# Kernel tuning notes

Measured on AMD Instinct MI355X. Metric: run time of the kernel, lower is better.

The kernel has to match this reference:

```python
import jax, jax.numpy as jnp
import numpy as np

T, B, D, H = 128, 64, 1024, 1024

def hard_sigmoid(x):
    # torch: clamp(x + 0.5, 0, 1)
    return jnp.clip(x + 0.5, 0.0, 1.0)

def hard_tanh(x):
    # torch F.hardtanh default: clamp(x, -1, 1)
    return jnp.clip(x, -1.0, 1.0)

def setup_inputs() -> dict:
    key = jax.random.key(0)
    k1, k2, k3 = jax.random.split(key, 3)
    scale = 1.0 / np.sqrt(H)
    x = jax.random.normal(k1, (T, B, D), dtype=jnp.float32)
    Wx = jax.random.normal(k2, (D, 4 * H), dtype=jnp.float32) * scale
    Wh = jax.random.normal(k3, (H, 4 * H), dtype=jnp.float32) * scale
    b = jnp.zeros((4 * H,), dtype=jnp.float32)
    return {"x": x, "Wx": Wx, "Wh": Wh, "b": b}

def reference(x, Wx, Wh, b):
    # Hard-LSTM cell unrolled over time (dim 0), state carried via lax.scan.
    Bsz = x.shape[1]
    Hd = Wh.shape[0]

    def step(carry, xt):
        h, c = carry
        gates = xt @ Wx + h @ Wh + b          # [B, 4H]
        i, f, g, o = jnp.split(gates, 4, axis=-1)
        i = hard_sigmoid(i)
        f = hard_sigmoid(f)
        g = hard_tanh(g)
        o = hard_sigmoid(o)
        c_new = f * c + i * g
        h_new = o * hard_tanh(c_new)
        return (h_new, c_new), h_new

    h0 = jnp.zeros((Bsz, Hd), dtype=x.dtype)
    c0 = jnp.zeros((Bsz, Hd), dtype=x.dtype)
    _, hs = jax.lax.scan(step, (h0, c0), x)   # hs: [T, B, H]
    return hs
```

## Files before the change

### kernel.cpp

```cpp
#include <hip/hip_runtime.h>

#define TT 128
#define BB 64
#define DD 1024
#define HH 1024
#define G4 4096
#define MM (TT*BB)
#define BH (BB*HH)

#define NWG 256
#define RPAD 520

typedef float f32x4 __attribute__((ext_vector_type(4)));

__device__ __forceinline__ float hsig(float x) {
    x += 0.5f;
    return fminf(fmaxf(x, 0.0f), 1.0f);
}
__device__ __forceinline__ float htanh(float x) {
    return fminf(fmaxf(x, -1.0f), 1.0f);
}

__global__ void zero_bar(unsigned* p) {
    p[threadIdx.x] = 0u;
}

__global__ __launch_bounds__(256) void gx_gemm(const float* __restrict__ X,
                                               const float* __restrict__ W,
                                               const float* __restrict__ bias,
                                               float* __restrict__ C) {
    __shared__ float As[16][132];
    __shared__ float Bs[16][132];

    const int tid = threadIdx.x;
    const int tx = tid & 15;
    const int ty = tid >> 4;
    const int m0 = blockIdx.y * 128;
    const int n0 = blockIdx.x * 128;

    float acc[8][8] = {};
    float4 ra[2], rb[2];

    #pragma unroll
    for (int i = 0; i < 2; ++i) {
        int f4 = tid + i * 256;
        ra[i] = *(const float4*)(X + (size_t)(m0 + (f4 >> 2)) * DD + (f4 & 3) * 4);
        rb[i] = *(const float4*)(W + (size_t)(f4 >> 5) * G4 + n0 + (f4 & 31) * 4);
    }

    for (int k0 = 0; k0 < DD; k0 += 16) {
        #pragma unroll
        for (int i = 0; i < 2; ++i) {
            int f4 = tid + i * 256;
            int mi = f4 >> 2, kq = f4 & 3;
            As[kq * 4 + 0][mi] = ra[i].x;
            As[kq * 4 + 1][mi] = ra[i].y;
            As[kq * 4 + 2][mi] = ra[i].z;
            As[kq * 4 + 3][mi] = ra[i].w;
            *(float4*)&Bs[f4 >> 5][(f4 & 31) * 4] = rb[i];
        }
        __syncthreads();

        const int kn = (k0 + 16 < DD) ? (k0 + 16) : k0;
        #pragma unroll
        for (int i = 0; i < 2; ++i) {
            int f4 = tid + i * 256;
            ra[i] = *(const float4*)(X + (size_t)(m0 + (f4 >> 2)) * DD + kn + (f4 & 3) * 4);
            rb[i] = *(const float4*)(W + (size_t)(kn + (f4 >> 5)) * G4 + n0 + (f4 & 31) * 4);
        }

        #pragma unroll
        for (int kk = 0; kk < 16; ++kk) {
            float ar[8], br[8];
            *(float4*)&ar[0] = *(const float4*)&As[kk][ty * 4];
            *(float4*)&ar[4] = *(const float4*)&As[kk][64 + ty * 4];
            *(float4*)&br[0] = *(const float4*)&Bs[kk][tx * 4];
            *(float4*)&br[4] = *(const float4*)&Bs[kk][64 + tx * 4];
            #pragma unroll
            for (int i = 0; i < 8; ++i)
                #pragma unroll
                for (int j = 0; j < 8; ++j)
                    acc[i][j] += ar[i] * br[j];
        }
        __syncthreads();
    }

    float bl[8];
    *(float4*)&bl[0] = *(const float4*)(bias + n0 + tx * 4);
    *(float4*)&bl[4] = *(const float4*)(bias + n0 + 64 + tx * 4);
    #pragma unroll
    for (int i = 0; i < 8; ++i) {
        int mrow = m0 + ty * 4 + (i & 3) + 64 * (i >> 2);
        float* crow = C + (size_t)mrow * G4 + n0;
        float4 o1, o2;
        o1.x = acc[i][0] + bl[0]; o1.y = acc[i][1] + bl[1];
        o1.z = acc[i][2] + bl[2]; o1.w = acc[i][3] + bl[3];
        o2.x = acc[i][4] + bl[4]; o2.y = acc[i][5] + bl[5];
        o2.z = acc[i][6] + bl[6]; o2.w = acc[i][7] + bl[7];
        *(float4*)(crow + tx * 4) = o1;
        *(float4*)(crow + 64 + tx * 4) = o2;
    }
}

__global__ __launch_bounds__(512) void lstm_persist(const float* __restrict__ Gx,
                                                    const float* __restrict__ Wh,
                                                    float* __restrict__ out,
                                                    unsigned* __restrict__ flags) {
    __shared__ float smem[16640 + 1024];
    float* hs   = smem;
    float* red  = smem;
    float* gsum = smem + 16640;

    const int tid   = threadIdx.x;
    const int btile = blockIdx.x >> 5;
    const int hct   = blockIdx.x & 31;
    const int b0  = btile * 8;
    const int hc0 = hct * 32;

    const int kc = tid >> 4;
    const int tt = tid & 15;
    const int gate_m = tt >> 2;
    const int sub8 = (tt & 3) * 8;
    const float* wbase = Wh + (size_t)(kc * 32) * G4 + gate_m * HH + hc0 + sub8;

    const int pp  = tid >> 4;
    const int ss  = tid & 15;
    const int srow = ss >> 1;
    const int cq0  = (ss & 1) * 4;

    const bool cell_act = (tid < 256);
    const int cb  = tid >> 5;
    const int chc = tid & 31;
    const size_t cell_g = (size_t)(b0 + cb) * G4 + hc0 + chc;
    const size_t cell_h = (size_t)(b0 + cb) * HH + hc0 + chc;
    float creg = 0.0f;

    const int rb_ = tid >> 7;
    const int rgc = tid & 127;
    const int rtt = rgc >> 3;
    const int rj  = rgc & 7;

    unsigned* gflags = flags + btile * 32;

    if (cell_act) {
        const float* gr = Gx + cell_g;
        float ii = hsig(gr[0]);
        float gv = htanh(gr[2 * HH]);
        float oo = hsig(gr[3 * HH]);
        creg = ii * gv;
        __hip_atomic_store(out + cell_h, oo * htanh(creg),
                           __ATOMIC_RELAXED, __HIP_MEMORY_SCOPE_AGENT);
    }
    asm volatile("s_waitcnt vmcnt(0)" ::: "memory");
    __syncthreads();
    if (tid == 0)
        __hip_atomic_store(gflags + hct, 1u, __ATOMIC_RELAXED,
                           __HIP_MEMORY_SCOPE_AGENT);

    for (int t = 1; t < TT; ++t) {
        float gi = 0.f, gf = 0.f, gg = 0.f, go = 0.f;
        if (cell_act) {
            const float* gr = Gx + (size_t)t * BB * G4 + cell_g;
            gi = gr[0];
            gf = gr[HH];
            gg = gr[2 * HH];
            go = gr[3 * HH];
        }

        {
            while (__hip_atomic_load(gflags + pp, __ATOMIC_RELAXED,
                                     __HIP_MEMORY_SCOPE_AGENT) < (unsigned)t)
                __builtin_amdgcn_s_sleep(1);

            const float* hp = out + (size_t)(t - 1) * BH
                            + (size_t)(b0 + srow) * HH + pp * 32 + cq0 * 4;
            f32x4 v0, v1, v2, v3;
            asm volatile(
                "global_load_dwordx4 %0, %4, off sc0\n\t"
                "global_load_dwordx4 %1, %4, off offset:16 sc0\n\t"
                "global_load_dwordx4 %2, %4, off offset:32 sc0\n\t"
                "global_load_dwordx4 %3, %4, off offset:48 sc0\n\t"
                "s_waitcnt vmcnt(0)"
                : "=&v"(v0), "=&v"(v1), "=&v"(v2), "=&v"(v3)
                : "v"(hp)
                : "memory");
            float* hd = &hs[srow * 1152 + pp * 36 + cq0 * 4];
            *(f32x4*)(hd)      = v0;
            *(f32x4*)(hd + 4)  = v1;
            *(f32x4*)(hd + 8)  = v2;
            *(f32x4*)(hd + 12) = v3;
        }
        __syncthreads();

        float acc[8][8] = {};
        const float* wp = wbase;
        #pragma unroll 2
        for (int k4 = 0; k4 < 8; ++k4) {
            f32x4 hv[8];
            #pragma unroll
            for (int bi = 0; bi < 8; ++bi)
                hv[bi] = *(const f32x4*)&hs[bi * 1152 + kc * 36 + k4 * 4];
            #pragma unroll
            for (int j = 0; j < 4; ++j) {
                f32x4 w0 = *(const f32x4*)(wp);
                f32x4 w1 = *(const f32x4*)(wp + 4);
                wp += G4;
                #pragma unroll
                for (int bi = 0; bi < 8; ++bi) {
                    float h = hv[bi][j];
                    acc[bi][0] += h * w0[0];
                    acc[bi][1] += h * w0[1];
                    acc[bi][2] += h * w0[2];
                    acc[bi][3] += h * w0[3];
                    acc[bi][4] += h * w1[0];
                    acc[bi][5] += h * w1[1];
                    acc[bi][6] += h * w1[2];
                    acc[bi][7] += h * w1[3];
                }
            }
        }
        __syncthreads();

        #pragma unroll
        for (int round = 0; round < 2; ++round) {
            #pragma unroll
            for (int bi = 0; bi < 4; ++bi)
                #pragma unroll
                for (int j = 0; j < 8; ++j)
                    red[(size_t)(bi * 8 + j) * RPAD + tid] = acc[round * 4 + bi][j];
            __syncthreads();
            {
                const float* rp = red + (size_t)(rb_ * 8 + rj) * RPAD + rtt;
                float s0 = 0.f, s1 = 0.f, s2 = 0.f, s3 = 0.f;
                #pragma unroll
                for (int k2 = 0; k2 < 32; k2 += 4) {
                    s0 += rp[(k2 + 0) * 16];
                    s1 += rp[(k2 + 1) * 16];
                    s2 += rp[(k2 + 2) * 16];
                    s3 += rp[(k2 + 3) * 16];
                }
                gsum[(round * 4 + rb_) * 128 + rgc] = (s0 + s1) + (s2 + s3);
            }
            __syncthreads();
        }

        if (cell_act) {
            float ii = hsig(gi + gsum[cb * 128 + chc]);
            float ff = hsig(gf + gsum[cb * 128 + 32 + chc]);
            float gv = htanh(gg + gsum[cb * 128 + 64 + chc]);
            float oo = hsig(go + gsum[cb * 128 + 96 + chc]);
            creg = ff * creg + ii * gv;
            __hip_atomic_store(out + (size_t)t * BH + cell_h, oo * htanh(creg),
                               __ATOMIC_RELAXED, __HIP_MEMORY_SCOPE_AGENT);
        }
        asm volatile("s_waitcnt vmcnt(0)" ::: "memory");
        __syncthreads();
        if (tid == 0)
            __hip_atomic_store(gflags + hct, (unsigned)(t + 1),
                               __ATOMIC_RELAXED, __HIP_MEMORY_SCOPE_AGENT);
    }
}

extern "C" void kernel_launch(void* const* d_in, const int* in_sizes, int n_in,
                              void* d_out, int out_size, void* d_ws, size_t ws_size,
                              hipStream_t stream) {
    const float* x  = (const float*)d_in[0];
    const float* Wx = (const float*)d_in[1];
    const float* Wh = (const float*)d_in[2];
    const float* bs = (const float*)d_in[3];
    float* out = (float*)d_out;

    float* Gx = (float*)d_ws;
    unsigned* flags = (unsigned*)(Gx + (size_t)MM * G4);

    zero_bar<<<dim3(1), dim3(256), 0, stream>>>(flags);

    gx_gemm<<<dim3(G4 / 128, MM / 128), dim3(256), 0, stream>>>(x, Wx, bs, Gx);

    lstm_persist<<<dim3(NWG), dim3(512), 0, stream>>>(Gx, Wh, out, flags);
}
```

Before: 2.470 ms.

## Prefetch Wh before flag spin, double-buffer K loop, merge reduction rounds

The first Wh tile is now loaded into registers before spinning on the producer flag, so weight fetch latency overlaps the cross-workgroup wait. The h-tile load is remapped so each wave reads only the hs slice it wrote itself. That lets a wave-local lgkmcnt wait replace the block-wide barrier. The K loop uses register double-buffering for both Wh and h fragments. The two-round LDS reduction becomes a single round over a doubled LDS buffer, removing two barriers per step. In exchange it raises VGPR and LDS pressure, which may limit scheduling or cause spills.

```diff
diff --git a/kernel.cpp b/kernel.cpp
--- a/kernel.cpp
+++ b/kernel.cpp
@@ -102,14 +102,44 @@
     }
 }
 
+#define LOADW(BUF, K4)                                                    \
+    {   const float* wn_ = wbase + (size_t)(K4) * 4 * G4;                 \
+        _Pragma("unroll")                                                 \
+        for (int j_ = 0; j_ < 4; ++j_) {                                  \
+            BUF[j_*2]   = *(const f32x4*)(wn_ + (size_t)j_ * G4);         \
+            BUF[j_*2+1] = *(const f32x4*)(wn_ + (size_t)j_ * G4 + 4);     \
+        } }
+
+#define LOADH(BUF, K4)                                                    \
+    {   _Pragma("unroll")                                                 \
+        for (int b_ = 0; b_ < 8; ++b_)                                    \
+            BUF[b_] = *(const f32x4*)&hs[b_ * 1152 + kc * 36 + (K4) * 4]; }
+
+#define FMA8(WB, HB)                                                      \
+    {   _Pragma("unroll")                                                 \
+        for (int j_ = 0; j_ < 4; ++j_) {                                  \
+            _Pragma("unroll")                                             \
+            for (int b_ = 0; b_ < 8; ++b_) {                              \
+                float h_ = HB[b_][j_];                                    \
+                acc[b_][0] += h_ * WB[j_*2][0];                           \
+                acc[b_][1] += h_ * WB[j_*2][1];                           \
+                acc[b_][2] += h_ * WB[j_*2][2];                           \
+                acc[b_][3] += h_ * WB[j_*2][3];                           \
+                acc[b_][4] += h_ * WB[j_*2+1][0];                         \
+                acc[b_][5] += h_ * WB[j_*2+1][1];                         \
+                acc[b_][6] += h_ * WB[j_*2+1][2];                         \
+                acc[b_][7] += h_ * WB[j_*2+1][3];                         \
+            } } }
+
 __global__ __launch_bounds__(512) void lstm_persist(const float* __restrict__ Gx,
                                                     const float* __restrict__ Wh,
                                                     float* __restrict__ out,
                                                     unsigned* __restrict__ flags) {
-    __shared__ float smem[16640 + 1024];
+    __shared__ float smem[2 * 16640 + 1024];
     float* hs   = smem;
-    float* red  = smem;
-    float* gsum = smem + 16640;
+    float* red0 = smem;
+    float* red1 = smem + 16640;
+    float* gsum = smem + 2 * 16640;
 
     const int tid   = threadIdx.x;
     const int btile = blockIdx.x >> 5;
@@ -123,10 +153,9 @@
     const int sub8 = (tt & 3) * 8;
     const float* wbase = Wh + (size_t)(kc * 32) * G4 + gate_m * HH + hc0 + sub8;
 
-    const int pp  = tid >> 4;
-    const int ss  = tid & 15;
-    const int srow = ss >> 1;
-    const int cq0  = (ss & 1) * 4;
+    const int pp  = kc;
+    const int srow = tt >> 1;
+    const int cq0  = (tt & 1) * 4;
 
     const bool cell_act = (tid < 256);
     const int cb  = tid >> 5;
@@ -167,11 +196,16 @@
             go = gr[3 * HH];
         }
 
+        float acc[8][8] = {};
+        f32x4 wb0[8], wb1[8], hv0[8], hv1[8];
+
+        LOADW(wb0, 0);
+
+        while (__hip_atomic_load(gflags + pp, __ATOMIC_RELAXED,
+                                 __HIP_MEMORY_SCOPE_AGENT) < (unsigned)t)
+            __builtin_amdgcn_s_sleep(1);
+
         {
-            while (__hip_atomic_load(gflags + pp, __ATOMIC_RELAXED,
-                                     __HIP_MEMORY_SCOPE_AGENT) < (unsigned)t)
-                __builtin_amdgcn_s_sleep(1);
-
             const float* hp = out + (size_t)(t - 1) * BH
                             + (size_t)(b0 + srow) * HH + pp * 32 + cq0 * 4;
             f32x4 v0, v1, v2, v3;
@@ -190,59 +224,51 @@
             *(f32x4*)(hd + 8)  = v2;
             *(f32x4*)(hd + 12) = v3;
         }
-        __syncthreads();
-
-        float acc[8][8] = {};
-        const float* wp = wbase;
-        #pragma unroll 2
-        for (int k4 = 0; k4 < 8; ++k4) {
-            f32x4 hv[8];
+        asm volatile("s_waitcnt lgkmcnt(0)" ::: "memory");
+        __builtin_amdgcn_sched_barrier(0);
+
+        LOADH(hv0, 0);
+        #pragma unroll 1
+        for (int kk = 0; kk < 4; ++kk) {
+            LOADW(wb1, kk * 2 + 1);
+            LOADH(hv1, kk * 2 + 1);
+            FMA8(wb0, hv0);
+            if (kk < 3) {
+                LOADW(wb0, kk * 2 + 2);
+                LOADH(hv0, kk * 2 + 2);
+            }
+            FMA8(wb1, hv1);
+        }
+        __syncthreads();
+
+        #pragma unroll
+        for (int bi = 0; bi < 4; ++bi)
             #pragma unroll
-            for (int bi = 0; bi < 8; ++bi)
-                hv[bi] = *(const f32x4*)&hs[bi * 1152 + kc * 36 + k4 * 4];
+            for (int j = 0; j < 8; ++j) {
+                red0[(size_t)(bi * 8 + j) * RPAD + tid] = acc[bi][j];
+                red1[(size_t)(bi * 8 + j) * RPAD + tid] = acc[4 + bi][j];
+            }
+        __syncthreads();
+        {
+            const float* rp0 = red0 + (size_t)(rb_ * 8 + rj) * RPAD + rtt;
+            const float* rp1 = red1 + (size_t)(rb_ * 8 + rj) * RPAD + rtt;
+            float a0 = 0.f, a1 = 0.f, a2 = 0.f, a3 = 0.f;
+            float c0 = 0.f, c1 = 0.f, c2 = 0.f, c3 = 0.f;
             #pragma unroll
-            for (int j = 0; j < 4; ++j) {
-                f32x4 w0 = *(const f32x4*)(wp);
-                f32x4 w1 = *(const f32x4*)(wp + 4);
-                wp += G4;
-                #pragma unroll
-                for (int bi = 0; bi < 8; ++bi) {
-                    float h = hv[bi][j];
-                    acc[bi][0] += h * w0[0];
-                    acc[bi][1] += h * w0[1];
-                    acc[bi][2] += h * w0[2];
-                    acc[bi][3] += h * w0[3];
-                    acc[bi][4] += h * w1[0];
-                    acc[bi][5] += h * w1[1];
-                    acc[bi][6] += h * w1[2];
-                    acc[bi][7] += h * w1[3];
-                }
+            for (int k2 = 0; k2 < 32; k2 += 4) {
+                a0 += rp0[(k2 + 0) * 16];
+                a1 += rp0[(k2 + 1) * 16];
+                a2 += rp0[(k2 + 2) * 16];
+                a3 += rp0[(k2 + 3) * 16];
+                c0 += rp1[(k2 + 0) * 16];
+                c1 += rp1[(k2 + 1) * 16];
+                c2 += rp1[(k2 + 2) * 16];
+                c3 += rp1[(k2 + 3) * 16];
             }
-        }
-        __syncthreads();
-
-        #pragma unroll
-        for (int round = 0; round < 2; ++round) {
-            #pragma unroll
-            for (int bi = 0; bi < 4; ++bi)
-                #pragma unroll
-                for (int j = 0; j < 8; ++j)
-                    red[(size_t)(bi * 8 + j) * RPAD + tid] = acc[round * 4 + bi][j];
-            __syncthreads();
-            {
-                const float* rp = red + (size_t)(rb_ * 8 + rj) * RPAD + rtt;
-                float s0 = 0.f, s1 = 0.f, s2 = 0.f, s3 = 0.f;
-                #pragma unroll
-                for (int k2 = 0; k2 < 32; k2 += 4) {
-                    s0 += rp[(k2 + 0) * 16];
-                    s1 += rp[(k2 + 1) * 16];
-                    s2 += rp[(k2 + 2) * 16];
-                    s3 += rp[(k2 + 3) * 16];
-                }
-                gsum[(round * 4 + rb_) * 128 + rgc] = (s0 + s1) + (s2 + s3);
-            }
-            __syncthreads();
-        }
+            gsum[rb_ * 128 + rgc]       = (a0 + a1) + (a2 + a3);
+            gsum[(4 + rb_) * 128 + rgc] = (c0 + c1) + (c2 + c3);
+        }
+        __syncthreads();
 
         if (cell_act) {
             float ii = hsig(gi + gsum[cb * 128 + chc]);
```

Measured after the change: 3.603 ms. 45.9% more time.

## Fuse input projection into persistent LSTM kernel, computing next step's x-gates after flag publish

Applied to the files above, without the earlier changes.

Removes the separate x@Wx GEMM kernel and its large Gx workspace. Each persistent workgroup now computes its own slice of x_t@Wx+b with the same FMA/reduce code as the recurrent part. It does this right after publishing h_t, so the work can overlap the wait for other workgroups' h. The trade-off is that every step now does twice the per-workgroup FMA work and streams Wx from memory each step, instead of using a bulk GEMM that runs once. Because the recurrence is latency-bound on the cross-workgroup flags, that extra work may hide in the idle time or may lengthen the critical path.

```diff
diff --git a/kernel.cpp b/kernel.cpp
--- a/kernel.cpp
+++ b/kernel.cpp
@@ -5,7 +5,6 @@
 #define DD 1024
 #define HH 1024
 #define G4 4096
-#define MM (TT*BB)
 #define BH (BB*HH)
 
 #define NWG 256
@@ -25,84 +24,88 @@
     p[threadIdx.x] = 0u;
 }
 
-__global__ __launch_bounds__(256) void gx_gemm(const float* __restrict__ X,
-                                               const float* __restrict__ W,
-                                               const float* __restrict__ bias,
-                                               float* __restrict__ C) {
-    __shared__ float As[16][132];
-    __shared__ float Bs[16][132];
-
-    const int tid = threadIdx.x;
-    const int tx = tid & 15;
-    const int ty = tid >> 4;
-    const int m0 = blockIdx.y * 128;
-    const int n0 = blockIdx.x * 128;
-
-    float acc[8][8] = {};
-    float4 ra[2], rb[2];
-
-    #pragma unroll
-    for (int i = 0; i < 2; ++i) {
-        int f4 = tid + i * 256;
-        ra[i] = *(const float4*)(X + (size_t)(m0 + (f4 >> 2)) * DD + (f4 & 3) * 4);
-        rb[i] = *(const float4*)(W + (size_t)(f4 >> 5) * G4 + n0 + (f4 & 31) * 4);
-    }
-
-    for (int k0 = 0; k0 < DD; k0 += 16) {
-        #pragma unroll
-        for (int i = 0; i < 2; ++i) {
-            int f4 = tid + i * 256;
-            int mi = f4 >> 2, kq = f4 & 3;
-            As[kq * 4 + 0][mi] = ra[i].x;
-            As[kq * 4 + 1][mi] = ra[i].y;
-            As[kq * 4 + 2][mi] = ra[i].z;
-            As[kq * 4 + 3][mi] = ra[i].w;
-            *(float4*)&Bs[f4 >> 5][(f4 & 31) * 4] = rb[i];
-        }
-        __syncthreads();
-
-        const int kn = (k0 + 16 < DD) ? (k0 + 16) : k0;
-        #pragma unroll
-        for (int i = 0; i < 2; ++i) {
-            int f4 = tid + i * 256;
-            ra[i] = *(const float4*)(X + (size_t)(m0 + (f4 >> 2)) * DD + kn + (f4 & 3) * 4);
-            rb[i] = *(const float4*)(W + (size_t)(kn + (f4 >> 5)) * G4 + n0 + (f4 & 31) * 4);
-        }
-
-        #pragma unroll
-        for (int kk = 0; kk < 16; ++kk) {
-            float ar[8], br[8];
-            *(float4*)&ar[0] = *(const float4*)&As[kk][ty * 4];
-            *(float4*)&ar[4] = *(const float4*)&As[kk][64 + ty * 4];
-            *(float4*)&br[0] = *(const float4*)&Bs[kk][tx * 4];
-            *(float4*)&br[4] = *(const float4*)&Bs[kk][64 + tx * 4];
-            #pragma unroll
-            for (int i = 0; i < 8; ++i)
-                #pragma unroll
-                for (int j = 0; j < 8; ++j)
-                    acc[i][j] += ar[i] * br[j];
-        }
-        __syncthreads();
-    }
-
-    float bl[8];
-    *(float4*)&bl[0] = *(const float4*)(bias + n0 + tx * 4);
-    *(float4*)&bl[4] = *(const float4*)(bias + n0 + 64 + tx * 4);
-    #pragma unroll
-    for (int i = 0; i < 8; ++i) {
-        int mrow = m0 + ty * 4 + (i & 3) + 64 * (i >> 2);
-        float* crow = C + (size_t)mrow * G4 + n0;
-        float4 o1, o2;
-        o1.x = acc[i][0] + bl[0]; o1.y = acc[i][1] + bl[1];
-        o1.z = acc[i][2] + bl[2]; o1.w = acc[i][3] + bl[3];
-        o2.x = acc[i][4] + bl[4]; o2.y = acc[i][5] + bl[5];
-        o2.z = acc[i][6] + bl[6]; o2.w = acc[i][7] + bl[7];
-        *(float4*)(crow + tx * 4) = o1;
-        *(float4*)(crow + 64 + tx * 4) = o2;
-    }
-}
-
-__global__ __launch_bounds__(512) void lstm_persist(const float* __restrict__ Gx,
+#define FMA_PHASE(WB)                                                      \
+    {   const float* wp = (WB);                                            \
+        _Pragma("unroll 2")                                                \
+        for (int k4 = 0; k4 < 8; ++k4) {                                   \
+            f32x4 hv[8];                                                   \
+            _Pragma("unroll")                                              \
+            for (int bi = 0; bi < 8; ++bi)                                 \
+                hv[bi] = *(const f32x4*)&hs[bi * 1152 + kc * 36 + k4 * 4]; \
+            _Pragma("unroll")                                              \
+            for (int j = 0; j < 4; ++j) {                                  \
+                f32x4 w0 = *(const f32x4*)(wp);                            \
+                f32x4 w1 = *(const f32x4*)(wp + 4);                        \
+                wp += G4;                                                  \
+                _Pragma("unroll")                                          \
+                for (int bi = 0; bi < 8; ++bi) {                           \
+                    float h = hv[bi][j];                                   \
+                    acc[bi][0] += h * w0[0];                               \
+                    acc[bi][1] += h * w0[1];                               \
+                    acc[bi][2] += h * w0[2];                               \
+                    acc[bi][3] += h * w0[3];                               \
+                    acc[bi][4] += h * w1[0];                               \
+                    acc[bi][5] += h * w1[1];                               \
+                    acc[bi][6] += h * w1[2];                               \
+                    acc[bi][7] += h * w1[3];                               \
+                } } } }
+
+#define REDUCE_PHASE()                                                     \
+    _Pragma("unroll")                                                      \
+    for (int round = 0; round < 2; ++round) {                              \
+        _Pragma("unroll")                                                  \
+        for (int bi = 0; bi < 4; ++bi)                                     \
+            _Pragma("unroll")                                              \
+            for (int j = 0; j < 8; ++j)                                    \
+                red[(size_t)(bi * 8 + j) * RPAD + tid] =                   \
+                    acc[round * 4 + bi][j];                                \
+        __syncthreads();                                                   \
+        {   const float* rp = red + (size_t)(rb_ * 8 + rj) * RPAD + rtt;   \
+            float s0 = 0.f, s1 = 0.f, s2 = 0.f, s3 = 0.f;                  \
+            _Pragma("unroll")                                              \
+            for (int k2 = 0; k2 < 32; k2 += 4) {                           \
+                s0 += rp[(k2 + 0) * 16];                                   \
+                s1 += rp[(k2 + 1) * 16];                                   \
+                s2 += rp[(k2 + 2) * 16];                                   \
+                s3 += rp[(k2 + 3) * 16];                                   \
+            }                                                              \
+            gsum[(round * 4 + rb_) * 128 + rgc] = (s0 + s1) + (s2 + s3);   \
+        }                                                                  \
+        __syncthreads();                                                   \
+    }
+
+#define STAGE_X(TIDX)                                                      \
+    {   const float* xr = X + ((size_t)(TIDX) * BB + b0 + xrow) * DD       \
+                        + xchunk * 16;                                     \
+        f32x4 a0 = *(const f32x4*)(xr);                                    \
+        f32x4 a1 = *(const f32x4*)(xr + 4);                                \
+        f32x4 a2 = *(const f32x4*)(xr + 8);                                \
+        f32x4 a3 = *(const f32x4*)(xr + 12);                               \
+        int k0_ = xchunk * 16;                                             \
+        float* xd = &hs[xrow * 1152 + (k0_ >> 5) * 36 + (k0_ & 31)];       \
+        *(f32x4*)(xd)      = a0;                                           \
+        *(f32x4*)(xd + 4)  = a1;                                           \
+        *(f32x4*)(xd + 8)  = a2;                                           \
+        *(f32x4*)(xd + 12) = a3;                                           \
+    }
+
+#define XGATES(TIDX)                                                       \
+    {   STAGE_X(TIDX);                                                     \
+        __syncthreads();                                                   \
+        float acc[8][8] = {};                                              \
+        FMA_PHASE(wbase_x);                                                \
+        __syncthreads();                                                   \
+        REDUCE_PHASE();                                                    \
+        if (cell_act) {                                                    \
+            xg[0] = gsum[cb * 128 + chc]      + bR[0];                     \
+            xg[1] = gsum[cb * 128 + 32 + chc] + bR[1];                     \
+            xg[2] = gsum[cb * 128 + 64 + chc] + bR[2];                     \
+            xg[3] = gsum[cb * 128 + 96 + chc] + bR[3];                     \
+        } }
+
+__global__ __launch_bounds__(512) void lstm_persist(const float* __restrict__ X,
+                                                    const float* __restrict__ Wx,
+                                                    const float* __restrict__ bias,
                                                     const float* __restrict__ Wh,
                                                     float* __restrict__ out,
                                                     unsigned* __restrict__ flags) {
@@ -121,17 +124,20 @@
     const int tt = tid & 15;
     const int gate_m = tt >> 2;
     const int sub8 = (tt & 3) * 8;
-    const float* wbase = Wh + (size_t)(kc * 32) * G4 + gate_m * HH + hc0 + sub8;
+    const float* wbase_h = Wh + (size_t)(kc * 32) * G4 + gate_m * HH + hc0 + sub8;
+    const float* wbase_x = Wx + (size_t)(kc * 32) * G4 + gate_m * HH + hc0 + sub8;
 
     const int pp  = tid >> 4;
     const int ss  = tid & 15;
     const int srow = ss >> 1;
     const int cq0  = (ss & 1) * 4;
 
+    const int xrow   = tid >> 6;
+    const int xchunk = tid & 63;
+
     const bool cell_act = (tid < 256);
     const int cb  = tid >> 5;
     const int chc = tid & 31;
-    const size_t cell_g = (size_t)(b0 + cb) * G4 + hc0 + chc;
     const size_t cell_h = (size_t)(b0 + cb) * HH + hc0 + chc;
     float creg = 0.0f;
 
@@ -142,11 +148,20 @@
 
     unsigned* gflags = flags + btile * 32;
 
+    float bR[4] = {0.f, 0.f, 0.f, 0.f};
+    float xg[4] = {0.f, 0.f, 0.f, 0.f};
     if (cell_act) {
-        const float* gr = Gx + cell_g;
-        float ii = hsig(gr[0]);
-        float gv = htanh(gr[2 * HH]);
-        float oo = hsig(gr[3 * HH]);
+        bR[0] = bias[hc0 + chc];
+        bR[1] = bias[HH + hc0 + chc];
+        bR[2] = bias[2 * HH + hc0 + chc];
+        bR[3] = bias[3 * HH + hc0 + chc];
+    }
+
+    XGATES(0);
+    if (cell_act) {
+        float ii = hsig(xg[0]);
+        float gv = htanh(xg[2]);
+        float oo = hsig(xg[3]);
         creg = ii * gv;
         __hip_atomic_store(out + cell_h, oo * htanh(creg),
                            __ATOMIC_RELAXED, __HIP_MEMORY_SCOPE_AGENT);
@@ -157,16 +172,9 @@
         __hip_atomic_store(gflags + hct, 1u, __ATOMIC_RELAXED,
                            __HIP_MEMORY_SCOPE_AGENT);
 
+    XGATES(1);
+
     for (int t = 1; t < TT; ++t) {
-        float gi = 0.f, gf = 0.f, gg = 0.f, go = 0.f;
-        if (cell_act) {
-            const float* gr = Gx + (size_t)t * BB * G4 + cell_g;
-            gi = gr[0];
-            gf = gr[HH];
-            gg = gr[2 * HH];
-            go = gr[3 * HH];
-        }
-
         {
             while (__hip_atomic_load(gflags + pp, __ATOMIC_RELAXED,
                                      __HIP_MEMORY_SCOPE_AGENT) < (unsigned)t)
@@ -192,63 +200,18 @@
         }
         __syncthreads();
 
-        float acc[8][8] = {};
-        const float* wp = wbase;
-        #pragma unroll 2
-        for (int k4 = 0; k4 < 8; ++k4) {
-            f32x4 hv[8];
-            #pragma unroll
-            for (int bi = 0; bi < 8; ++bi)
-                hv[bi] = *(const f32x4*)&hs[bi * 1152 + kc * 36 + k4 * 4];
-            #pragma unroll
-            for (int j = 0; j < 4; ++j) {
-                f32x4 w0 = *(const f32x4*)(wp);
-                f32x4 w1 = *(const f32x4*)(wp + 4);
-                wp += G4;
-                #pragma unroll
-                for (int bi = 0; bi < 8; ++bi) {
-                    float h = hv[bi][j];
-                    acc[bi][0] += h * w0[0];
-                    acc[bi][1] += h * w0[1];
-                    acc[bi][2] += h * w0[2];
-                    acc[bi][3] += h * w0[3];
-                    acc[bi][4] += h * w1[0];
-                    acc[bi][5] += h * w1[1];
-                    acc[bi][6] += h * w1[2];
-                    acc[bi][7] += h * w1[3];
-                }
-            }
-        }
-        __syncthreads();
-
-        #pragma unroll
-        for (int round = 0; round < 2; ++round) {
-            #pragma unroll
-            for (int bi = 0; bi < 4; ++bi)
-                #pragma unroll
-                for (int j = 0; j < 8; ++j)
-                    red[(size_t)(bi * 8 + j) * RPAD + tid] = acc[round * 4 + bi][j];
+        {
+            float acc[8][8] = {};
+            FMA_PHASE(wbase_h);
             __syncthreads();
-            {
-                const float* rp = red + (size_t)(rb_ * 8 + rj) * RPAD + rtt;
-                float s0 = 0.f, s1 = 0.f, s2 = 0.f, s3 = 0.f;
-                #pragma unroll
-                for (int k2 = 0; k2 < 32; k2 += 4) {
-                    s0 += rp[(k2 + 0) * 16];
-                    s1 += rp[(k2 + 1) * 16];
-                    s2 += rp[(k2 + 2) * 16];
-                    s3 += rp[(k2 + 3) * 16];
-                }
-                gsum[(round * 4 + rb_) * 128 + rgc] = (s0 + s1) + (s2 + s3);
-            }
-            __syncthreads();
+            REDUCE_PHASE();
         }
 
         if (cell_act) {
-            float ii = hsig(gi + gsum[cb * 128 + chc]);
-            float ff = hsig(gf + gsum[cb * 128 + 32 + chc]);
-            float gv = htanh(gg + gsum[cb * 128 + 64 + chc]);
-            float oo = hsig(go + gsum[cb * 128 + 96 + chc]);
+            float ii = hsig(xg[0] + gsum[cb * 128 + chc]);
+            float ff = hsig(xg[1] + gsum[cb * 128 + 32 + chc]);
+            float gv = htanh(xg[2] + gsum[cb * 128 + 64 + chc]);
+            float oo = hsig(xg[3] + gsum[cb * 128 + 96 + chc]);
             creg = ff * creg + ii * gv;
             __hip_atomic_store(out + (size_t)t * BH + cell_h, oo * htanh(creg),
                                __ATOMIC_RELAXED, __HIP_MEMORY_SCOPE_AGENT);
@@ -258,6 +221,10 @@
         if (tid == 0)
             __hip_atomic_store(gflags + hct, (unsigned)(t + 1),
                                __ATOMIC_RELAXED, __HIP_MEMORY_SCOPE_AGENT);
+
+        if (t < TT - 1) {
+            XGATES(t + 1);
+        }
     }
 }
 
@@ -270,12 +237,10 @@
     const float* bs = (const float*)d_in[3];
     float* out = (float*)d_out;
 
-    float* Gx = (float*)d_ws;
-    unsigned* flags = (unsigned*)(Gx + (size_t)MM * G4);
+    unsigned* flags = (unsigned*)d_ws;
 
     zero_bar<<<dim3(1), dim3(256), 0, stream>>>(flags);
 
-    gx_gemm<<<dim3(G4 / 128, MM / 128), dim3(256), 0, stream>>>(x, Wx, bs, Gx);
-
-    lstm_persist<<<dim3(NWG), dim3(512), 0, stream>>>(Gx, Wh, out, flags);
-}
+    lstm_persist<<<dim3(NWG), dim3(512), 0, stream>>>(x, Wx, bs, Wh, out,
+                                                      flags);
+}
```

New measurement: 2.772 ms. +12.2%, slower.

## Use per-wavefront readiness flags and single-round double-buffered reduction

Applied to the files above, without the earlier changes.

Each wavefront that writes h now publishes its own flag after its stores complete, so the end-of-step __syncthreads and single-thread flag store go away. Consumers poll only the flag covering the two batch rows they read. The cross-thread reduction now fills two LDS buffers at once, which removes one of the two barrier rounds per step. LDS use roughly doubles, which may lower occupancy, and the flag array grows, so the zeroing kernel now launches 1024 threads.

```diff
diff --git a/kernel.cpp b/kernel.cpp
--- a/kernel.cpp
+++ b/kernel.cpp
@@ -106,10 +106,11 @@
                                                     const float* __restrict__ Wh,
                                                     float* __restrict__ out,
                                                     unsigned* __restrict__ flags) {
-    __shared__ float smem[16640 + 1024];
+    __shared__ float smem[2 * 16640 + 1024];
     float* hs   = smem;
-    float* red  = smem;
-    float* gsum = smem + 16640;
+    float* red0 = smem;
+    float* red1 = smem + 16640;
+    float* gsum = smem + 2 * 16640;
 
     const int tid   = threadIdx.x;
     const int btile = blockIdx.x >> 5;
@@ -140,7 +141,9 @@
     const int rtt = rgc >> 3;
     const int rj  = rgc & 7;
 
-    unsigned* gflags = flags + btile * 32;
+    unsigned* bflags = flags + btile * 128;
+    unsigned* pollp  = bflags + pp * 4 + (srow >> 1);
+    unsigned* myflag = bflags + hct * 4 + (tid >> 6);
 
     if (cell_act) {
         const float* gr = Gx + cell_g;
@@ -150,12 +153,11 @@
         creg = ii * gv;
         __hip_atomic_store(out + cell_h, oo * htanh(creg),
                            __ATOMIC_RELAXED, __HIP_MEMORY_SCOPE_AGENT);
-    }
-    asm volatile("s_waitcnt vmcnt(0)" ::: "memory");
-    __syncthreads();
-    if (tid == 0)
-        __hip_atomic_store(gflags + hct, 1u, __ATOMIC_RELAXED,
-                           __HIP_MEMORY_SCOPE_AGENT);
+        asm volatile("s_waitcnt vmcnt(0)" ::: "memory");
+        if ((tid & 63) == 0)
+            __hip_atomic_store(myflag, 1u, __ATOMIC_RELAXED,
+                               __HIP_MEMORY_SCOPE_AGENT);
+    }
 
     for (int t = 1; t < TT; ++t) {
         float gi = 0.f, gf = 0.f, gg = 0.f, go = 0.f;
@@ -168,7 +170,7 @@
         }
 
         {
-            while (__hip_atomic_load(gflags + pp, __ATOMIC_RELAXED,
+            while (__hip_atomic_load(pollp, __ATOMIC_RELAXED,
                                      __HIP_MEMORY_SCOPE_AGENT) < (unsigned)t)
                 __builtin_amdgcn_s_sleep(1);
 
@@ -222,27 +224,33 @@
         __syncthreads();
 
         #pragma unroll
-        for (int round = 0; round < 2; ++round) {
-            #pragma unroll
-            for (int bi = 0; bi < 4; ++bi)
-                #pragma unroll
-                for (int j = 0; j < 8; ++j)
-                    red[(size_t)(bi * 8 + j) * RPAD + tid] = acc[round * 4 + bi][j];
-            __syncthreads();
-            {
-                const float* rp = red + (size_t)(rb_ * 8 + rj) * RPAD + rtt;
-                float s0 = 0.f, s1 = 0.f, s2 = 0.f, s3 = 0.f;
-                #pragma unroll
-                for (int k2 = 0; k2 < 32; k2 += 4) {
-                    s0 += rp[(k2 + 0) * 16];
-                    s1 += rp[(k2 + 1) * 16];
-                    s2 += rp[(k2 + 2) * 16];
-                    s3 += rp[(k2 + 3) * 16];
-                }
-                gsum[(round * 4 + rb_) * 128 + rgc] = (s0 + s1) + (s2 + s3);
+        for (int bi = 0; bi < 4; ++bi)
+            #pragma unroll
+            for (int j = 0; j < 8; ++j) {
+                red0[(size_t)(bi * 8 + j) * RPAD + tid] = acc[bi][j];
+                red1[(size_t)(bi * 8 + j) * RPAD + tid] = acc[4 + bi][j];
             }
-            __syncthreads();
-        }
+        __syncthreads();
+        {
+            const float* rp0 = red0 + (size_t)(rb_ * 8 + rj) * RPAD + rtt;
+            const float* rp1 = red1 + (size_t)(rb_ * 8 + rj) * RPAD + rtt;
+            float a0 = 0.f, a1 = 0.f, a2 = 0.f, a3 = 0.f;
+            float c0 = 0.f, c1 = 0.f, c2 = 0.f, c3 = 0.f;
+            #pragma unroll
+            for (int k2 = 0; k2 < 32; k2 += 4) {
+                a0 += rp0[(k2 + 0) * 16];
+                a1 += rp0[(k2 + 1) * 16];
+                a2 += rp0[(k2 + 2) * 16];
+                a3 += rp0[(k2 + 3) * 16];
+                c0 += rp1[(k2 + 0) * 16];
+                c1 += rp1[(k2 + 1) * 16];
+                c2 += rp1[(k2 + 2) * 16];
+                c3 += rp1[(k2 + 3) * 16];
+            }
+            gsum[rb_ * 128 + rgc]       = (a0 + a1) + (a2 + a3);
+            gsum[(4 + rb_) * 128 + rgc] = (c0 + c1) + (c2 + c3);
+        }
+        __syncthreads();
 
         if (cell_act) {
             float ii = hsig(gi + gsum[cb * 128 + chc]);
@@ -252,12 +260,11 @@
             creg = ff * creg + ii * gv;
             __hip_atomic_store(out + (size_t)t * BH + cell_h, oo * htanh(creg),
                                __ATOMIC_RELAXED, __HIP_MEMORY_SCOPE_AGENT);
-        }
-        asm volatile("s_waitcnt vmcnt(0)" ::: "memory");
-        __syncthreads();
-        if (tid == 0)
-            __hip_atomic_store(gflags + hct, (unsigned)(t + 1),
-                               __ATOMIC_RELAXED, __HIP_MEMORY_SCOPE_AGENT);
+            asm volatile("s_waitcnt vmcnt(0)" ::: "memory");
+            if ((tid & 63) == 0)
+                __hip_atomic_store(myflag, (unsigned)(t + 1), __ATOMIC_RELAXED,
+                                   __HIP_MEMORY_SCOPE_AGENT);
+        }
     }
 }
 
@@ -273,7 +280,7 @@
     float* Gx = (float*)d_ws;
     unsigned* flags = (unsigned*)(Gx + (size_t)MM * G4);
 
-    zero_bar<<<dim3(1), dim3(256), 0, stream>>>(flags);
+    zero_bar<<<dim3(1), dim3(1024), 0, stream>>>(flags);
 
     gx_gemm<<<dim3(G4 / 128, MM / 128), dim3(256), 0, stream>>>(x, Wx, bs, Gx);
 
```

Measured after the change: 2.362 ms. 1.05x faster.
